# Performance work log

Hardware: AMD Instinct MI355X
Metric: run time of the kernel (lower is better)

## Reference

```python
import jax, jax.numpy as jnp
import numpy as np

N = 20000      # nodes
E = 160000     # edges
F_IN = 128     # node_feature_dim
HID = 128      # hidden_dim
HEADS = 8
G = 64         # graphs in batch


def setup_inputs() -> dict:
    key = jax.random.key(0)
    ks = iter(jax.random.split(key, 40))

    def w(shape, fan):
        return jax.random.normal(next(ks), shape, jnp.float32) / np.sqrt(fan)

    inp = {}
    inp['x'] = jax.random.normal(next(ks), (N, F_IN), jnp.float32)
    inp['edge_index'] = jax.random.randint(next(ks), (2, E), 0, N, jnp.int32)
    inp['batch'] = jnp.sort(jax.random.randint(next(ks), (N,), 0, G, jnp.int32))
    # initial projection
    inp['Wp'] = w((F_IN, HID), F_IN); inp['bp'] = jnp.zeros((HID,), jnp.float32)
    # layers 0..2: TransformerConv(HID -> HID//HEADS per head, heads=HEADS, concat) => heads*out = HID
    inp['Wq'] = w((3, HID, HID), HID); inp['bq'] = jnp.zeros((3, HID), jnp.float32)
    inp['Wk'] = w((3, HID, HID), HID); inp['bk'] = jnp.zeros((3, HID), jnp.float32)
    inp['Wv'] = w((3, HID, HID), HID); inp['bv'] = jnp.zeros((3, HID), jnp.float32)
    inp['Ws'] = w((3, HID, HID), HID); inp['bs'] = jnp.zeros((3, HID), jnp.float32)
    inp['Wbeta'] = w((3, 3 * HID, 1), 3 * HID)
    # layer 3: TransformerConv(HID -> HID per head, heads=HEADS, concat=False -> head mean)
    inp['Wq3'] = w((HID, HEADS * HID), HID); inp['bq3'] = jnp.zeros((HEADS * HID,), jnp.float32)
    inp['Wk3'] = w((HID, HEADS * HID), HID); inp['bk3'] = jnp.zeros((HEADS * HID,), jnp.float32)
    inp['Wv3'] = w((HID, HEADS * HID), HID); inp['bv3'] = jnp.zeros((HEADS * HID,), jnp.float32)
    inp['Ws3'] = w((HID, HID), HID); inp['bs3'] = jnp.zeros((HID,), jnp.float32)
    inp['Wbeta3'] = w((3 * HID, 1), 3 * HID)
    # batchnorm affine params for 4 layers
    inp['bn_gamma'] = jnp.ones((4, HID), jnp.float32)
    inp['bn_beta'] = jnp.zeros((4, HID), jnp.float32)
    return inp


def _tconv(x, src, dst, Wq, bq, Wk, bk, Wv, bv, Ws, bs, Wb, heads, concat):
    n = x.shape[0]
    d = Wq.shape[1] // heads  # per-head dim
    q = (x @ Wq + bq).reshape(n, heads, d)
    k = (x @ Wk + bk).reshape(n, heads, d)
    v = (x @ Wv + bv).reshape(n, heads, d)
    # per-edge attention logits [E, heads]
    logits = jnp.einsum('ehd,ehd->eh', q[dst], k[src]) / jnp.sqrt(jnp.float32(d))
    # segment softmax over incoming edges of each target node
    m = jax.ops.segment_max(logits, dst, num_segments=n)
    m = jnp.where(jnp.isfinite(m), m, 0.0)
    ex = jnp.exp(logits - m[dst])
    denom = jax.ops.segment_sum(ex, dst, num_segments=n)
    a = ex / (denom[dst] + 1e-16)  # [E, heads]
    out = jax.ops.segment_sum(a[:, :, None] * v[src], dst, num_segments=n)  # [n, heads, d]
    out = out.reshape(n, heads * d) if concat else out.mean(axis=1)
    # beta-gated skip connection
    r = x @ Ws + bs
    g = jax.nn.sigmoid(jnp.concatenate([out, r, out - r], axis=-1) @ Wb)  # [n, 1]
    return g * r + (1.0 - g) * out


def _bn(x, gamma, beta):
    mu = x.mean(axis=0)
    var = x.var(axis=0)
    return (x - mu) * jax.lax.rsqrt(var + 1e-5) * gamma + beta


def reference(x, edge_index, batch, Wp, bp, Wq, bq, Wk, bk, Wv, bv, Ws, bs, Wbeta,
              Wq3, bq3, Wk3, bk3, Wv3, bv3, Ws3, bs3, Wbeta3, bn_gamma, bn_beta):
    src, dst = edge_index[0], edge_index[1]
    h = x @ Wp + bp
    for i in range(3):
        h = _tconv(h, src, dst, Wq[i], bq[i], Wk[i], bk[i], Wv[i], bv[i],
                   Ws[i], bs[i], Wbeta[i], HEADS, concat=True)
        h = jax.nn.relu(_bn(h, bn_gamma[i], bn_beta[i]))
    h = _tconv(h, src, dst, Wq3, bq3, Wk3, bk3, Wv3, bv3, Ws3, bs3, Wbeta3,
               HEADS, concat=False)
    h = jax.nn.relu(_bn(h, bn_gamma[3], bn_beta[3]))
    # global mean pool per graph
    sums = jax.ops.segment_sum(h, batch, num_segments=G)
    cnt = jax.ops.segment_sum(jnp.ones((h.shape[0],), h.dtype), batch, num_segments=G)
    return sums / jnp.maximum(cnt, 1.0)[:, None]
```

## Files before the change

### kernel.cpp

```cpp
#include <hip/hip_runtime.h>
#include <math.h>

#define NNODES 20000
#define NPAD   20096
#define NEDGES 160000
#define HIDDIM 128
#define NHEADS 8
#define NGRAPH 64
#define KC 384
#define GXTILES 157

typedef short short8 __attribute__((ext_vector_type(8)));
typedef float floatx4 __attribute__((ext_vector_type(4)));
typedef unsigned short ushort4v __attribute__((ext_vector_type(4)));

__device__ inline unsigned short f2bf(float x) {
    unsigned u = __float_as_uint(x);
    u += 0x7fff + ((u >> 16) & 1);
    return (unsigned short)(u >> 16);
}
__device__ inline float bf2f(unsigned short h) {
    return __uint_as_float(((unsigned)h) << 16);
}

__device__ __forceinline__ void gload16(const unsigned short* g, unsigned short* l) {
    __builtin_amdgcn_global_load_lds(
        (const __attribute__((address_space(1))) unsigned int*)g,
        (__attribute__((address_space(3))) unsigned int*)l, 16, 0, 0);
}

__global__ __launch_bounds__(256) void zero_kernel(float* __restrict__ p, int n) {
    int i = blockIdx.x * blockDim.x + threadIdx.x;
    if (i < n) p[i] = 0.f;
}

__global__ __launch_bounds__(256) void count_deg_kernel(const int* __restrict__ dst,
                                                        int* __restrict__ deg, int e) {
    int i = blockIdx.x * blockDim.x + threadIdx.x;
    if (i < e) atomicAdd(&deg[dst[i]], 1);
}

__global__ __launch_bounds__(256) void scan1_kernel(const int* __restrict__ deg,
                                                    int* __restrict__ chunk,
                                                    int* __restrict__ bsum, int n) {
    __shared__ int buf[256];
    int t = threadIdx.x;
    int i = blockIdx.x * 256 + t;
    int v = (i < n) ? deg[i] : 0;
    buf[t] = v;
    __syncthreads();
    for (int off = 1; off < 256; off <<= 1) {
        int tmp = (t >= off) ? buf[t - off] : 0;
        __syncthreads();
        buf[t] += tmp;
        __syncthreads();
    }
    if (i < n) chunk[i] = buf[t];
    if (t == 255) bsum[blockIdx.x] = buf[255];
}

__global__ __launch_bounds__(128) void scan2_kernel(int* __restrict__ bsum, int nb) {
    __shared__ int buf[128];
    int t = threadIdx.x;
    int v = (t < nb) ? bsum[t] : 0;
    buf[t] = v;
    __syncthreads();
    for (int off = 1; off < 128; off <<= 1) {
        int tmp = (t >= off) ? buf[t - off] : 0;
        __syncthreads();
        buf[t] += tmp;
        __syncthreads();
    }
    if (t < nb) bsum[t] = buf[t] - v;
}

__global__ __launch_bounds__(256) void scan3_kernel(const int* __restrict__ chunk,
                                                    const int* __restrict__ bsum,
                                                    int* __restrict__ offs, int n) {
    int i = blockIdx.x * 256 + threadIdx.x;
    if (i < n) offs[i + 1] = chunk[i] + bsum[i >> 8];
    if (i == 0) offs[0] = 0;
}

__global__ __launch_bounds__(256) void scatter_kernel(const int* __restrict__ src,
                                                      const int* __restrict__ dst,
                                                      const int* __restrict__ offs,
                                                      int* __restrict__ cursor,
                                                      int* __restrict__ csr_src, int e) {
    int i = blockIdx.x * blockDim.x + threadIdx.x;
    if (i < e) {
        int d = dst[i];
        int pos = offs[d] + atomicAdd(&cursor[d], 1);
        csr_src[pos] = src[i];
    }
}

__global__ __launch_bounds__(128) void prep_w_kernel(
    const float* __restrict__ Wq, const float* __restrict__ Wk,
    const float* __restrict__ Wv, const float* __restrict__ Ws,
    const float* __restrict__ Wp, const float* __restrict__ Ws3,
    unsigned short* __restrict__ WtAll) {
    int id = blockIdx.x;
    int k = threadIdx.x;
    float w;
    if (id < 1536) {
        int li = id / 512, n = id % 512, sel = n >> 7, np = n & 127;
        const float* W = (sel == 0) ? Wq : (sel == 1) ? Wk : (sel == 2) ? Wv : Ws;
        w = W[li * 16384 + k * 128 + np];
    } else if (id < 1664) {
        w = Wp[k * 128 + (id - 1536)];
    } else if (id < 2688) {
        return;
    } else {
        w = Ws3[k * 128 + (id - 2688)];
    }
    unsigned short hi = f2bf(w);
    unsigned short lo = f2bf(w - bf2f(hi));
    unsigned short* dst = WtAll + (size_t)id * KC;
    dst[k] = hi;
    dst[128 + k] = hi;
    dst[256 + k] = lo;
}

__global__ __launch_bounds__(256) void prep_bias_kernel(
    const float* __restrict__ bq, const float* __restrict__ bk,
    const float* __restrict__ bv, const float* __restrict__ bs,
    const float* __restrict__ bs3, float* __restrict__ bcat) {
    int id = blockIdx.x * 256 + threadIdx.x;
    if (id >= 2688) return;
    float v;
    if (id < 1536) {
        int li = id / 512, n = id % 512, sel = n >> 7, np = n & 127;
        const float* b = (sel == 0) ? bq : (sel == 1) ? bk : (sel == 2) ? bv : bs;
        v = b[li * 128 + np];
    } else if (id < 2560) {
        return;
    } else {
        v = bs3[id - 2560];
    }
    bcat[id] = v;
}

__global__ __launch_bounds__(128) void mqk_kernel(
    const float* __restrict__ Wq3, const float* __restrict__ Wk3,
    const float* __restrict__ bq3,
    unsigned short* __restrict__ WtAll, float* __restrict__ bcat) {
    int hb = blockIdx.x;
    int h = hb >> 7, b = hb & 127;
    int a = threadIdx.x;
    __shared__ float wk[128];
    wk[a] = Wk3[(size_t)b * 1024 + h * 128 + a];
    __syncthreads();
    const float* wq = Wq3 + (size_t)a * 1024 + h * 128;
    float acc = 0.f;
#pragma unroll 16
    for (int d = 0; d < 128; ++d) acc = fmaf(wq[d], wk[d], acc);
    unsigned short hi = f2bf(acc);
    unsigned short lo = f2bf(acc - bf2f(hi));
    unsigned short* dst = WtAll + (size_t)(1664 + h * 128 + b) * KC;
    dst[a] = hi;
    dst[128 + a] = hi;
    dst[256 + a] = lo;
    if (a == 0) {
        float bb = 0.f;
        for (int d = 0; d < 128; ++d) bb = fmaf(bq3[h * 128 + d], wk[d], bb);
        bcat[1536 + h * 128 + b] = bb;
    }
}

__global__ __launch_bounds__(128) void prep_wvm_kernel(
    const float* __restrict__ Wv3, const float* __restrict__ bv3,
    unsigned short* __restrict__ Wvm, float* __restrict__ bvm) {
    int j = blockIdx.x;
    int a = threadIdx.x;
#pragma unroll
    for (int h = 0; h < 8; ++h) {
        float w = Wv3[(size_t)a * 1024 + h * 128 + j] * 0.125f;
        Wvm[(size_t)j * 1024 + h * 128 + a] = f2bf(w);
    }
    if (a == 0) {
        float s = 0.f;
        for (int h = 0; h < 8; ++h) s += bv3[h * 128 + j];
        bvm[j] = s * 0.125f;
    }
}

__global__ __launch_bounds__(256) void cat_from_kernel(const float* __restrict__ h,
                                                       unsigned short* __restrict__ Acat) {
    int idx = blockIdx.x * 256 + threadIdx.x;
    if (idx >= NPAD * HIDDIM) return;
    int r = idx >> 7, k = idx & 127;
    float x = (r < NNODES) ? h[idx] : 0.f;
    unsigned short hi = f2bf(x);
    unsigned short lo = f2bf(x - bf2f(hi));
    unsigned short* row = Acat + (size_t)r * KC;
    row[k] = hi;
    row[128 + k] = lo;
    row[256 + k] = hi;
}

template <typename OutT, int KG, int BY, int ST>
__global__ __launch_bounds__(256) void gemm_lds_kernel(
    const unsigned short* __restrict__ A, const unsigned short* __restrict__ Wt,
    const float* __restrict__ bias, OutT* __restrict__ C, int M, int nrows) {
    int id = blockIdx.x;
    int xcd = id & 7;
    int idx = id >> 3;
    int bx = (idx / BY) * 8 + xcd;
    int by = idx % BY;
    if (bx >= GXTILES) return;

    __shared__ unsigned short lds[2][2][4096];

    int tid = threadIdx.x;
    int lane = tid & 63;
    int wave = tid >> 6;
    int m = lane & 15;
    int q = lane >> 4;
    int nodeBase = bx * 128 + (wave & 1) * 64;
    int featBase = by * 128 + (wave >> 1) * 64;

    const unsigned short* gA = A + (size_t)bx * 128 * ST;
    const unsigned short* gW = Wt + (size_t)by * 128 * ST;

    int rs = lane >> 2;
    int cp0 = lane & 3;

    auto stagef = [&](int buf, int kk) {
        int kof = kk * 32;
#pragma unroll
        for (int jj = 0; jj < 2; ++jj) {
            int j = wave * 2 + jj;
            int row = j * 16 + rs;
            int g = cp0 ^ ((row >> 1) & 3);
            gload16(gA + (size_t)row * ST + kof + g * 8,
                    &lds[buf][0][0] + (size_t)j * 512);
            gload16(gW + (size_t)row * ST + kof + g * 8,
                    &lds[buf][1][0] + (size_t)j * 512);
        }
    };

    floatx4 acc[4][4];
#pragma unroll
    for (int r = 0; r < 4; ++r)
#pragma unroll
        for (int c = 0; c < 4; ++c) acc[r][c] = (floatx4){0.f, 0.f, 0.f, 0.f};

    stagef(0, 0);
    __syncthreads();

    for (int kg = 0; kg < KG; ++kg) {
        int cur = kg & 1;
        if (kg + 1 < KG) stagef(cur ^ 1, kg + 1);
        short8 a[4], b[4];
#pragma unroll
        for (int r = 0; r < 4; ++r) {
            int wr = (wave >> 1) * 64 + r * 16 + m;
            int cp = q ^ ((wr >> 1) & 3);
            a[r] = *(const short8*)(&lds[cur][1][0] + wr * 32 + cp * 8);
        }
#pragma unroll
        for (int c = 0; c < 4; ++c) {
            int ar = (wave & 1) * 64 + c * 16 + m;
            int cp = q ^ ((ar >> 1) & 3);
            b[c] = *(const short8*)(&lds[cur][0][0] + ar * 32 + cp * 8);
        }
#pragma unroll
        for (int r = 0; r < 4; ++r)
#pragma unroll
            for (int c = 0; c < 4; ++c)
                acc[r][c] = __builtin_amdgcn_mfma_f32_16x16x32_bf16(a[r], b[c], acc[r][c], 0, 0, 0);
        __syncthreads();
    }

    float4 bv[4];
#pragma unroll
    for (int r = 0; r < 4; ++r) bv[r] = *(const float4*)(bias + featBase + r * 16 + q * 4);
#pragma unroll
    for (int c = 0; c < 4; ++c) {
        int node = nodeBase + c * 16 + m;
        if (node < nrows) {
#pragma unroll
            for (int r = 0; r < 4; ++r) {
                int f0 = featBase + r * 16 + q * 4;
                float v0 = acc[r][c][0] + bv[r].x;
                float v1 = acc[r][c][1] + bv[r].y;
                float v2 = acc[r][c][2] + bv[r].z;
                float v3 = acc[r][c][3] + bv[r].w;
                if (sizeof(OutT) == 2) {
                    ushort4v o = {f2bf(v0), f2bf(v1), f2bf(v2), f2bf(v3)};
                    *(ushort4v*)((unsigned short*)C + (size_t)node * M + f0) = o;
                } else {
                    float4 o = {v0, v1, v2, v3};
                    *(float4*)((float*)C + (size_t)node * M + f0) = o;
                }
            }
        }
    }
}

__global__ __launch_bounds__(64) void attn_small_kernel(
    const unsigned short* __restrict__ qkvs,
    const float* __restrict__ Wb,
    const int* __restrict__ offs, const int* __restrict__ csr_src,
    float* __restrict__ out) {
    int i = blockIdx.x;
    int l = threadIdx.x;
    int g = l >> 5;
    int d0 = (l & 31) * 4;
    uint2 qraw = *(const uint2*)(qkvs + (size_t)i * 512 + d0);
    float q0 = bf2f((unsigned short)(qraw.x & 0xffff)), q1 = bf2f((unsigned short)(qraw.x >> 16));
    float q2 = bf2f((unsigned short)(qraw.y & 0xffff)), q3 = bf2f((unsigned short)(qraw.y >> 16));
    int e0 = offs[i], e1 = offs[i + 1];
    float lac = 0.f;
    float a0 = 0.f, a1 = 0.f, a2 = 0.f, a3 = 0.f;
    for (int e = e0 + g; e < e1; e += 2) {
        int sn = csr_src[e];
        const unsigned short* row = qkvs + (size_t)sn * 512;
        uint2 kk = *(const uint2*)(row + 128 + d0);
        uint2 vv = *(const uint2*)(row + 256 + d0);
        float k0 = bf2f((unsigned short)(kk.x & 0xffff)), k1 = bf2f((unsigned short)(kk.x >> 16));
        float k2 = bf2f((unsigned short)(kk.y & 0xffff)), k3 = bf2f((unsigned short)(kk.y >> 16));
        float p = q0 * k0 + q1 * k1 + q2 * k2 + q3 * k3;
        p += __shfl_xor(p, 1);
        p += __shfl_xor(p, 2);
        float w = __expf(p * 0.25f);
        float v0 = bf2f((unsigned short)(vv.x & 0xffff)), v1 = bf2f((unsigned short)(vv.x >> 16));
        float v2 = bf2f((unsigned short)(vv.y & 0xffff)), v3 = bf2f((unsigned short)(vv.y >> 16));
        a0 += w * v0;
        a1 += w * v1;
        a2 += w * v2;
        a3 += w * v3;
        lac += w;
    }
    a0 += __shfl_xor(a0, 32);
    a1 += __shfl_xor(a1, 32);
    a2 += __shfl_xor(a2, 32);
    a3 += __shfl_xor(a3, 32);
    lac += __shfl_xor(lac, 32);
    float inv = 1.f / (lac + 1e-16f);
    float o0 = a0 * inv, o1 = a1 * inv, o2 = a2 * inv, o3 = a3 * inv;
    uint2 rraw = *(const uint2*)(qkvs + (size_t)i * 512 + 384 + d0);
    float r0 = bf2f((unsigned short)(rraw.x & 0xffff)), r1 = bf2f((unsigned short)(rraw.x >> 16));
    float r2 = bf2f((unsigned short)(rraw.y & 0xffff)), r3 = bf2f((unsigned short)(rraw.y >> 16));
    float part = o0 * Wb[d0] + o1 * Wb[d0 + 1] + o2 * Wb[d0 + 2] + o3 * Wb[d0 + 3]
               + r0 * Wb[128 + d0] + r1 * Wb[128 + d0 + 1]
               + r2 * Wb[128 + d0 + 2] + r3 * Wb[128 + d0 + 3]
               + (o0 - r0) * Wb[256 + d0] + (o1 - r1) * Wb[256 + d0 + 1]
               + (o2 - r2) * Wb[256 + d0 + 2] + (o3 - r3) * Wb[256 + d0 + 3];
    if (g) part = 0.f;
#pragma unroll
    for (int msk = 1; msk <= 32; msk <<= 1) part += __shfl_xor(part, msk);
    float gg = 1.f / (1.f + __expf(-part));
    if (g == 0) {
        float4 o4 = {gg * r0 + (1.f - gg) * o0, gg * r1 + (1.f - gg) * o1,
                     gg * r2 + (1.f - gg) * o2, gg * r3 + (1.f - gg) * o3};
        *(float4*)(out + (size_t)i * HIDDIM + d0) = o4;
    }
}

__global__ __launch_bounds__(64) void attn_big_kernel(
    const unsigned short* __restrict__ tbuf, const unsigned short* __restrict__ Acat,
    const int* __restrict__ offs, const int* __restrict__ csr_src,
    unsigned short* __restrict__ agg) {
    int i = blockIdx.x;
    int l = threadIdx.x;
    int doff = (l & 7) * 16;
    const unsigned short* tp = tbuf + (size_t)i * 1152 + l * 16;
    uint4 t0 = *(const uint4*)tp;
    uint4 t1 = *(const uint4*)(tp + 8);
    float tq[16];
    tq[0] = bf2f((unsigned short)(t0.x & 0xffff)); tq[1] = bf2f((unsigned short)(t0.x >> 16));
    tq[2] = bf2f((unsigned short)(t0.y & 0xffff)); tq[3] = bf2f((unsigned short)(t0.y >> 16));
    tq[4] = bf2f((unsigned short)(t0.z & 0xffff)); tq[5] = bf2f((unsigned short)(t0.z >> 16));
    tq[6] = bf2f((unsigned short)(t0.w & 0xffff)); tq[7] = bf2f((unsigned short)(t0.w >> 16));
    tq[8] = bf2f((unsigned short)(t1.x & 0xffff)); tq[9] = bf2f((unsigned short)(t1.x >> 16));
    tq[10] = bf2f((unsigned short)(t1.y & 0xffff)); tq[11] = bf2f((unsigned short)(t1.y >> 16));
    tq[12] = bf2f((unsigned short)(t1.z & 0xffff)); tq[13] = bf2f((unsigned short)(t1.z >> 16));
    tq[14] = bf2f((unsigned short)(t1.w & 0xffff)); tq[15] = bf2f((unsigned short)(t1.w >> 16));
    int e0 = offs[i], e1 = offs[i + 1];
    float ac[16];
#pragma unroll
    for (int j = 0; j < 16; ++j) ac[j] = 0.f;
    float lac = 0.f;
    for (int e = e0; e < e1; ++e) {
        int sn = csr_src[e];
        const unsigned short* hp = Acat + (size_t)sn * KC + doff;
        uint4 k0 = *(const uint4*)hp;
        uint4 k1 = *(const uint4*)(hp + 8);
        float kk[16];
        kk[0] = bf2f((unsigned short)(k0.x & 0xffff)); kk[1] = bf2f((unsigned short)(k0.x >> 16));
        kk[2] = bf2f((unsigned short)(k0.y & 0xffff)); kk[3] = bf2f((unsigned short)(k0.y >> 16));
        kk[4] = bf2f((unsigned short)(k0.z & 0xffff)); kk[5] = bf2f((unsigned short)(k0.z >> 16));
        kk[6] = bf2f((unsigned short)(k0.w & 0xffff)); kk[7] = bf2f((unsigned short)(k0.w >> 16));
        kk[8] = bf2f((unsigned short)(k1.x & 0xffff)); kk[9] = bf2f((unsigned short)(k1.x >> 16));
        kk[10] = bf2f((unsigned short)(k1.y & 0xffff)); kk[11] = bf2f((unsigned short)(k1.y >> 16));
        kk[12] = bf2f((unsigned short)(k1.z & 0xffff)); kk[13] = bf2f((unsigned short)(k1.z >> 16));
        kk[14] = bf2f((unsigned short)(k1.w & 0xffff)); kk[15] = bf2f((unsigned short)(k1.w >> 16));
        float p = 0.f;
#pragma unroll
        for (int j = 0; j < 16; ++j) p = fmaf(tq[j], kk[j], p);
        p += __shfl_xor(p, 1);
        p += __shfl_xor(p, 2);
        p += __shfl_xor(p, 4);
        float w = __expf(p * 0.08838834764831845f);
#pragma unroll
        for (int j = 0; j < 16; ++j) ac[j] = fmaf(w, kk[j], ac[j]);
        lac += w;
    }
    float inv = 1.f / (lac + 1e-16f);
    unsigned short* o = agg + (size_t)i * 1024 + l * 16;
    ushort4v o0 = {f2bf(ac[0] * inv), f2bf(ac[1] * inv), f2bf(ac[2] * inv), f2bf(ac[3] * inv)};
    ushort4v o1 = {f2bf(ac[4] * inv), f2bf(ac[5] * inv), f2bf(ac[6] * inv), f2bf(ac[7] * inv)};
    ushort4v o2 = {f2bf(ac[8] * inv), f2bf(ac[9] * inv), f2bf(ac[10] * inv), f2bf(ac[11] * inv)};
    ushort4v o3 = {f2bf(ac[12] * inv), f2bf(ac[13] * inv), f2bf(ac[14] * inv), f2bf(ac[15] * inv)};
    *(ushort4v*)o = o0;
    *(ushort4v*)(o + 4) = o1;
    *(ushort4v*)(o + 8) = o2;
    *(ushort4v*)(o + 12) = o3;
}

__global__ __launch_bounds__(128) void beta3_kernel(const float* __restrict__ omean,
                                                    const unsigned short* __restrict__ tbuf,
                                                    const float* __restrict__ Wb,
                                                    float* __restrict__ out) {
    int i = blockIdx.x, t = threadIdx.x;
    float o = omean[(size_t)i * HIDDIM + t];
    float r = bf2f(tbuf[(size_t)i * 1152 + 1024 + t]);
    float part = o * Wb[t] + r * Wb[128 + t] + (o - r) * Wb[256 + t];
#pragma unroll
    for (int msk = 1; msk <= 32; msk <<= 1) part += __shfl_xor(part, msk);
    __shared__ float wsum[2];
    if ((t & 63) == 0) wsum[t >> 6] = part;
    __syncthreads();
    float tot = wsum[0] + wsum[1];
    float g = 1.f / (1.f + __expf(-tot));
    out[(size_t)i * HIDDIM + t] = g * r + (1.f - g) * o;
}

__global__ __launch_bounds__(128) void bn_stats_kernel(const float* __restrict__ x,
                                                       float* __restrict__ stat, int n) {
    int t = threadIdx.x;
    float s = 0.f, sq = 0.f;
    for (int i = blockIdx.x; i < n; i += gridDim.x) {
        float v = x[(size_t)i * HIDDIM + t];
        s += v;
        sq += v * v;
    }
    atomicAdd(&stat[t], s);
    atomicAdd(&stat[HIDDIM + t], sq);
}

__global__ __launch_bounds__(128) void bn_apply_kernel(float* __restrict__ x,
                                                       const float* __restrict__ stat,
                                                       const float* __restrict__ gamma,
                                                       const float* __restrict__ beta, int n,
                                                       unsigned short* __restrict__ cat) {
    int t = threadIdx.x;
    float mu = stat[t] / (float)n;
    float var = stat[HIDDIM + t] / (float)n - mu * mu;
    float rs = rsqrtf(var + 1e-5f);
    float g = gamma[t], b = beta[t];
    for (int i = blockIdx.x; i < n; i += gridDim.x) {
        float v = x[(size_t)i * HIDDIM + t];
        v = fmaxf((v - mu) * rs * g + b, 0.f);
        x[(size_t)i * HIDDIM + t] = v;
        if (cat) {
            unsigned short hi = f2bf(v);
            unsigned short lo = f2bf(v - bf2f(hi));
            unsigned short* row = cat + (size_t)i * KC;
            row[t] = hi;
            row[128 + t] = lo;
            row[256 + t] = hi;
        }
    }
}

__global__ __launch_bounds__(256) void gb_kernel(const int* __restrict__ batch,
                                                 int* __restrict__ gs,
                                                 int* __restrict__ ge, int n) {
    int i = blockIdx.x * 256 + threadIdx.x;
    if (i >= n) return;
    int b = batch[i];
    if (i == 0 || batch[i - 1] != b) gs[b] = i;
    if (i == n - 1 || batch[i + 1] != b) ge[b] = i + 1;
}

__global__ __launch_bounds__(256) void pool_part_kernel(const float* __restrict__ x,
                                                        const int* __restrict__ gs,
                                                        const int* __restrict__ ge,
                                                        float* __restrict__ out) {
    int g = blockIdx.x, c = blockIdx.y;
    int t = threadIdx.x;
    int f = t & 127, half = t >> 7;
    int s = gs[g], e = ge[g];
    float acc = 0.f;
    for (int i = s + 2 * c + half; i < e; i += 16) acc += x[(size_t)i * HIDDIM + f];
    __shared__ float l0[128];
    if (half == 0) l0[f] = acc;
    __syncthreads();
    if (half == 1) atomicAdd(&out[g * HIDDIM + f], l0[f] + acc);
}

__global__ __launch_bounds__(128) void pool_div_kernel(float* __restrict__ out,
                                                       const int* __restrict__ gs,
                                                       const int* __restrict__ ge) {
    int g = blockIdx.x, t = threadIdx.x;
    int c = ge[g] - gs[g];
    out[g * HIDDIM + t] /= (float)(c > 0 ? c : 1);
}

extern "C" void kernel_launch(void* const* d_in, const int* in_sizes, int n_in,
                              void* d_out, int out_size, void* d_ws, size_t ws_size,
                              hipStream_t stream) {
    const float* x       = (const float*)d_in[0];
    const int*   ei      = (const int*)d_in[1];
    const int*   batch   = (const int*)d_in[2];
    const float* Wp      = (const float*)d_in[3];
    const float* bp      = (const float*)d_in[4];
    const float* Wq      = (const float*)d_in[5];
    const float* bq      = (const float*)d_in[6];
    const float* Wk      = (const float*)d_in[7];
    const float* bk      = (const float*)d_in[8];
    const float* Wv      = (const float*)d_in[9];
    const float* bv      = (const float*)d_in[10];
    const float* Ws      = (const float*)d_in[11];
    const float* bs      = (const float*)d_in[12];
    const float* Wbeta   = (const float*)d_in[13];
    const float* Wq3     = (const float*)d_in[14];
    const float* bq3     = (const float*)d_in[15];
    const float* Wk3     = (const float*)d_in[16];
    const float* bk3     = (const float*)d_in[17];
    const float* Wv3     = (const float*)d_in[18];
    const float* bv3     = (const float*)d_in[19];
    const float* Ws3     = (const float*)d_in[20];
    const float* bs3     = (const float*)d_in[21];
    const float* Wbeta3  = (const float*)d_in[22];
    const float* bn_gamma = (const float*)d_in[23];
    const float* bn_beta  = (const float*)d_in[24];
    float* out = (float*)d_out;
    (void)bk3;

    const int* esrc = ei;
    const int* edst = ei + NEDGES;

    char* wpc = (char*)d_ws;
    auto alloc = [&](size_t nbytes) -> char* {
        char* p = wpc;
        wpc += (nbytes + 255) & ~(size_t)255;
        return p;
    };
    unsigned short* Acat  = (unsigned short*)alloc((size_t)NPAD * KC * 2);
    unsigned short* WtAll = (unsigned short*)alloc((size_t)2816 * KC * 2);
    float* bcat   = (float*)alloc(2688 * 4);
    unsigned short* Wvm   = (unsigned short*)alloc((size_t)128 * 1024 * 2);
    float* bvm    = (float*)alloc(128 * 4);
    unsigned short* tbuf  = (unsigned short*)alloc((size_t)NPAD * 1152 * 2);
    unsigned short* aggb  = (unsigned short*)alloc((size_t)NPAD * 1024 * 2);
    float* omean  = (float*)alloc((size_t)NNODES * HIDDIM * 4);
    float* hbuf   = (float*)alloc((size_t)NNODES * HIDDIM * 4);
    float* obuf   = (float*)alloc((size_t)NNODES * HIDDIM * 4);
    int*   deg    = (int*)alloc((2 * NNODES + 128 + 4 * 256) * 4);
    int*   cursor = deg + NNODES;
    int*   gs     = deg + 2 * NNODES;
    int*   ge     = gs + NGRAPH;
    float* bnstat4 = (float*)(deg + 2 * NNODES + 128);
    int*   chunk  = (int*)alloc(NNODES * 4);
    int*   bsum   = (int*)alloc(128 * 4);
    int*   offs   = (int*)alloc((NNODES + 1) * 4);
    int*   csrsrc = (int*)alloc(NEDGES * 4);

    unsigned short* WtQKVS = WtAll;
    unsigned short* Wpt    = WtAll + (size_t)1536 * KC;
    unsigned short* Wt3    = WtAll + (size_t)1664 * KC;
    float* bQKVS = bcat;
    float* b3    = bcat + 1536;
    unsigned short* qkvs = tbuf;

    const int TB = 256;
    const int ZWORDS = 2 * NNODES + 128 + 4 * 256;
    zero_kernel<<<(ZWORDS + TB - 1) / TB, TB, 0, stream>>>((float*)deg, ZWORDS);
    count_deg_kernel<<<(NEDGES + TB - 1) / TB, TB, 0, stream>>>(edst, deg, NEDGES);
    const int NB = (NNODES + 255) / 256;
    scan1_kernel<<<NB, 256, 0, stream>>>(deg, chunk, bsum, NNODES);
    scan2_kernel<<<1, 128, 0, stream>>>(bsum, NB);
    scan3_kernel<<<NB, 256, 0, stream>>>(chunk, bsum, offs, NNODES);
    scatter_kernel<<<(NEDGES + TB - 1) / TB, TB, 0, stream>>>(esrc, edst, offs, cursor, csrsrc, NEDGES);
    gb_kernel<<<(NNODES + TB - 1) / TB, TB, 0, stream>>>(batch, gs, ge, NNODES);

    prep_w_kernel<<<2816, 128, 0, stream>>>(Wq, Wk, Wv, Ws, Wp, Ws3, WtAll);
    prep_bias_kernel<<<(2688 + TB - 1) / TB, TB, 0, stream>>>(bq, bk, bv, bs, bs3, bcat);
    mqk_kernel<<<1024, 128, 0, stream>>>(Wq3, Wk3, bq3, WtAll, bcat);
    prep_wvm_kernel<<<128, 128, 0, stream>>>(Wv3, bv3, Wvm, bvm);

    const int CATB = (NPAD * HIDDIM + TB - 1) / TB;
    const int GSW = 8 * ((GXTILES + 7) / 8);

    cat_from_kernel<<<CATB, TB, 0, stream>>>(x, Acat);
    gemm_lds_kernel<float, 12, 1, KC><<<GSW * 1, 256, 0, stream>>>(Acat, Wpt, bp, hbuf, 128, NNODES);
    cat_from_kernel<<<CATB, TB, 0, stream>>>(hbuf, Acat);

    for (int li = 0; li < 3; ++li) {
        gemm_lds_kernel<unsigned short, 8, 4, KC><<<GSW * 4, 256, 0, stream>>>(
            Acat, WtQKVS + (size_t)li * 512 * KC, bQKVS + li * 512, qkvs, 512, NNODES);
        attn_small_kernel<<<NNODES, 64, 0, stream>>>(qkvs, Wbeta + li * 384,
                                                     offs, csrsrc, obuf);
        float* st = bnstat4 + li * 256;
        bn_stats_kernel<<<640, 128, 0, stream>>>(obuf, st, NNODES);
        bn_apply_kernel<<<512, 128, 0, stream>>>(obuf, st, bn_gamma + li * HIDDIM,
                                                 bn_beta + li * HIDDIM, NNODES, Acat);
    }

    gemm_lds_kernel<unsigned short, 8, 9, KC><<<GSW * 9, 256, 0, stream>>>(
        Acat, Wt3, b3, tbuf, 1152, NNODES);
    attn_big_kernel<<<NNODES, 64, 0, stream>>>(tbuf, Acat, offs, csrsrc, aggb);
    gemm_lds_kernel<float, 32, 1, 1024><<<GSW, 256, 0, stream>>>(
        aggb, Wvm, bvm, omean, HIDDIM, NNODES);
    beta3_kernel<<<NNODES, 128, 0, stream>>>(omean, tbuf, Wbeta3, hbuf);
    float* st3 = bnstat4 + 3 * 256;
    bn_stats_kernel<<<640, 128, 0, stream>>>(hbuf, st3, NNODES);
    bn_apply_kernel<<<512, 128, 0, stream>>>(hbuf, st3, bn_gamma + 3 * HIDDIM,
                                             bn_beta + 3 * HIDDIM, NNODES, (unsigned short*)0);

    zero_kernel<<<(NGRAPH * HIDDIM + TB - 1) / TB, TB, 0, stream>>>(out, NGRAPH * HIDDIM);
    pool_part_kernel<<<dim3(NGRAPH, 8), 256, 0, stream>>>(hbuf, gs, ge, out);
    pool_div_kernel<<<NGRAPH, 128, 0, stream>>>(out, gs, ge);
}
```

Baseline: 513.1 us.

## Fuse setup, epilogue, BN stats and pooling kernels to cut launches and passes

Merges several small kernels: scatter with graph-boundary detection, the bias prep into the weight prep, mqk with the Wv3 mean prep, and the final beta gate with BN statistics accumulation. BN apply, ReLU and mean pooling are folded into one per-graph kernel. The projection GEMM now writes the split bf16 hi/lo activation layout directly, which removes a cat_from pass. Launch count and several full passes over node features go down. In exchange, pooling runs with only 64 blocks, and the BN statistics rely on a zeroed stat buffer plus float atomics and E[x^2]-mu^2 variance.

```diff
diff --git a/kernel.cpp b/kernel.cpp
--- a/kernel.cpp
+++ b/kernel.cpp
@@ -82,26 +82,50 @@
     if (i == 0) offs[0] = 0;
 }
 
-__global__ __launch_bounds__(256) void scatter_kernel(const int* __restrict__ src,
-                                                      const int* __restrict__ dst,
-                                                      const int* __restrict__ offs,
-                                                      int* __restrict__ cursor,
-                                                      int* __restrict__ csr_src, int e) {
+__global__ __launch_bounds__(256) void scatter_gb_kernel(
+    const int* __restrict__ src, const int* __restrict__ dst,
+    const int* __restrict__ offs, int* __restrict__ cursor,
+    int* __restrict__ csr_src, int e,
+    const int* __restrict__ batch, int* __restrict__ gs, int* __restrict__ ge, int n) {
     int i = blockIdx.x * blockDim.x + threadIdx.x;
     if (i < e) {
         int d = dst[i];
         int pos = offs[d] + atomicAdd(&cursor[d], 1);
         csr_src[pos] = src[i];
     }
+    if (i < n) {
+        int b = batch[i];
+        if (i == 0 || batch[i - 1] != b) gs[b] = i;
+        if (i == n - 1 || batch[i + 1] != b) ge[b] = i + 1;
+    }
 }
 
 __global__ __launch_bounds__(128) void prep_w_kernel(
     const float* __restrict__ Wq, const float* __restrict__ Wk,
     const float* __restrict__ Wv, const float* __restrict__ Ws,
     const float* __restrict__ Wp, const float* __restrict__ Ws3,
-    unsigned short* __restrict__ WtAll) {
+    const float* __restrict__ bq, const float* __restrict__ bk,
+    const float* __restrict__ bv, const float* __restrict__ bs,
+    const float* __restrict__ bs3,
+    unsigned short* __restrict__ WtAll, float* __restrict__ bcat) {
     int id = blockIdx.x;
     int k = threadIdx.x;
+    if (id >= 2816) {
+        int idx = (id - 2816) * 128 + k;
+        if (idx >= 2688) return;
+        float v;
+        if (idx < 1536) {
+            int li = idx / 512, n = idx % 512, sel = n >> 7, np = n & 127;
+            const float* b = (sel == 0) ? bq : (sel == 1) ? bk : (sel == 2) ? bv : bs;
+            v = b[li * 128 + np];
+        } else if (idx < 2560) {
+            return;
+        } else {
+            v = bs3[idx - 2560];
+        }
+        bcat[idx] = v;
+        return;
+    }
     float w;
     if (id < 1536) {
         int li = id / 512, n = id % 512, sel = n >> 7, np = n & 127;
@@ -122,32 +146,29 @@
     dst[256 + k] = lo;
 }
 
-__global__ __launch_bounds__(256) void prep_bias_kernel(
-    const float* __restrict__ bq, const float* __restrict__ bk,
-    const float* __restrict__ bv, const float* __restrict__ bs,
-    const float* __restrict__ bs3, float* __restrict__ bcat) {
-    int id = blockIdx.x * 256 + threadIdx.x;
-    if (id >= 2688) return;
-    float v;
-    if (id < 1536) {
-        int li = id / 512, n = id % 512, sel = n >> 7, np = n & 127;
-        const float* b = (sel == 0) ? bq : (sel == 1) ? bk : (sel == 2) ? bv : bs;
-        v = b[li * 128 + np];
-    } else if (id < 2560) {
-        return;
-    } else {
-        v = bs3[id - 2560];
-    }
-    bcat[id] = v;
-}
-
-__global__ __launch_bounds__(128) void mqk_kernel(
+__global__ __launch_bounds__(128) void mqk_wvm_kernel(
     const float* __restrict__ Wq3, const float* __restrict__ Wk3,
     const float* __restrict__ bq3,
-    unsigned short* __restrict__ WtAll, float* __restrict__ bcat) {
+    const float* __restrict__ Wv3, const float* __restrict__ bv3,
+    unsigned short* __restrict__ WtAll, float* __restrict__ bcat,
+    unsigned short* __restrict__ Wvm, float* __restrict__ bvm) {
+    int a = threadIdx.x;
+    if (blockIdx.x >= 1024) {
+        int j = blockIdx.x - 1024;
+#pragma unroll
+        for (int h = 0; h < 8; ++h) {
+            float w = Wv3[(size_t)a * 1024 + h * 128 + j] * 0.125f;
+            Wvm[(size_t)j * 1024 + h * 128 + a] = f2bf(w);
+        }
+        if (a == 0) {
+            float s = 0.f;
+            for (int h = 0; h < 8; ++h) s += bv3[h * 128 + j];
+            bvm[j] = s * 0.125f;
+        }
+        return;
+    }
     int hb = blockIdx.x;
     int h = hb >> 7, b = hb & 127;
-    int a = threadIdx.x;
     __shared__ float wk[128];
     wk[a] = Wk3[(size_t)b * 1024 + h * 128 + a];
     __syncthreads();
@@ -168,23 +189,6 @@
     }
 }
 
-__global__ __launch_bounds__(128) void prep_wvm_kernel(
-    const float* __restrict__ Wv3, const float* __restrict__ bv3,
-    unsigned short* __restrict__ Wvm, float* __restrict__ bvm) {
-    int j = blockIdx.x;
-    int a = threadIdx.x;
-#pragma unroll
-    for (int h = 0; h < 8; ++h) {
-        float w = Wv3[(size_t)a * 1024 + h * 128 + j] * 0.125f;
-        Wvm[(size_t)j * 1024 + h * 128 + a] = f2bf(w);
-    }
-    if (a == 0) {
-        float s = 0.f;
-        for (int h = 0; h < 8; ++h) s += bv3[h * 128 + j];
-        bvm[j] = s * 0.125f;
-    }
-}
-
 __global__ __launch_bounds__(256) void cat_from_kernel(const float* __restrict__ h,
                                                        unsigned short* __restrict__ Acat) {
     int idx = blockIdx.x * 256 + threadIdx.x;
@@ -199,7 +203,7 @@
     row[256 + k] = hi;
 }
 
-template <typename OutT, int KG, int BY, int ST>
+template <typename OutT, int KG, int BY, int ST, int OMODE>
 __global__ __launch_bounds__(256) void gemm_lds_kernel(
     const unsigned short* __restrict__ A, const unsigned short* __restrict__ Wt,
     const float* __restrict__ bias, OutT* __restrict__ C, int M, int nrows) {
@@ -287,7 +291,16 @@
                 float v1 = acc[r][c][1] + bv[r].y;
                 float v2 = acc[r][c][2] + bv[r].z;
                 float v3 = acc[r][c][3] + bv[r].w;
-                if (sizeof(OutT) == 2) {
+                if (OMODE == 2) {
+                    unsigned short* row = (unsigned short*)C + (size_t)node * KC;
+                    unsigned short h0 = f2bf(v0), h1 = f2bf(v1), h2 = f2bf(v2), h3 = f2bf(v3);
+                    ushort4v hiv = {h0, h1, h2, h3};
+                    ushort4v lov = {f2bf(v0 - bf2f(h0)), f2bf(v1 - bf2f(h1)),
+                                    f2bf(v2 - bf2f(h2)), f2bf(v3 - bf2f(h3))};
+                    *(ushort4v*)(row + f0) = hiv;
+                    *(ushort4v*)(row + 128 + f0) = lov;
+                    *(ushort4v*)(row + 256 + f0) = hiv;
+                } else if (OMODE == 1) {
                     ushort4v o = {f2bf(v0), f2bf(v1), f2bf(v2), f2bf(v3)};
                     *(ushort4v*)((unsigned short*)C + (size_t)node * M + f0) = o;
                 } else {
@@ -420,22 +433,31 @@
     *(ushort4v*)(o + 12) = o3;
 }
 
-__global__ __launch_bounds__(128) void beta3_kernel(const float* __restrict__ omean,
-                                                    const unsigned short* __restrict__ tbuf,
-                                                    const float* __restrict__ Wb,
-                                                    float* __restrict__ out) {
-    int i = blockIdx.x, t = threadIdx.x;
-    float o = omean[(size_t)i * HIDDIM + t];
-    float r = bf2f(tbuf[(size_t)i * 1152 + 1024 + t]);
-    float part = o * Wb[t] + r * Wb[128 + t] + (o - r) * Wb[256 + t];
-#pragma unroll
-    for (int msk = 1; msk <= 32; msk <<= 1) part += __shfl_xor(part, msk);
+__global__ __launch_bounds__(128) void beta3_stats_kernel(
+    const float* __restrict__ omean, const unsigned short* __restrict__ tbuf,
+    const float* __restrict__ Wb, float* __restrict__ out,
+    float* __restrict__ stat, int n) {
+    int t = threadIdx.x;
     __shared__ float wsum[2];
-    if ((t & 63) == 0) wsum[t >> 6] = part;
-    __syncthreads();
-    float tot = wsum[0] + wsum[1];
-    float g = 1.f / (1.f + __expf(-tot));
-    out[(size_t)i * HIDDIM + t] = g * r + (1.f - g) * o;
+    float s = 0.f, sq = 0.f;
+    for (int i = blockIdx.x; i < n; i += gridDim.x) {
+        float o = omean[(size_t)i * HIDDIM + t];
+        float r = bf2f(tbuf[(size_t)i * 1152 + 1024 + t]);
+        float part = o * Wb[t] + r * Wb[128 + t] + (o - r) * Wb[256 + t];
+#pragma unroll
+        for (int msk = 1; msk <= 32; msk <<= 1) part += __shfl_xor(part, msk);
+        if ((t & 63) == 0) wsum[t >> 6] = part;
+        __syncthreads();
+        float tot = wsum[0] + wsum[1];
+        __syncthreads();
+        float g = 1.f / (1.f + __expf(-tot));
+        float v = g * r + (1.f - g) * o;
+        out[(size_t)i * HIDDIM + t] = v;
+        s += v;
+        sq += v * v;
+    }
+    atomicAdd(&stat[t], s);
+    atomicAdd(&stat[HIDDIM + t], sq);
 }
 
 __global__ __launch_bounds__(128) void bn_stats_kernel(const float* __restrict__ x,
@@ -476,38 +498,29 @@
     }
 }
 
-__global__ __launch_bounds__(256) void gb_kernel(const int* __restrict__ batch,
-                                                 int* __restrict__ gs,
-                                                 int* __restrict__ ge, int n) {
-    int i = blockIdx.x * 256 + threadIdx.x;
-    if (i >= n) return;
-    int b = batch[i];
-    if (i == 0 || batch[i - 1] != b) gs[b] = i;
-    if (i == n - 1 || batch[i + 1] != b) ge[b] = i + 1;
-}
-
-__global__ __launch_bounds__(256) void pool_part_kernel(const float* __restrict__ x,
-                                                        const int* __restrict__ gs,
-                                                        const int* __restrict__ ge,
-                                                        float* __restrict__ out) {
-    int g = blockIdx.x, c = blockIdx.y;
+__global__ __launch_bounds__(256) void pool_bn_kernel(
+    const float* __restrict__ x, const float* __restrict__ stat,
+    const float* __restrict__ gamma, const float* __restrict__ beta,
+    const int* __restrict__ gs, const int* __restrict__ ge,
+    float* __restrict__ out, int n) {
+    int g = blockIdx.x;
     int t = threadIdx.x;
     int f = t & 127, half = t >> 7;
+    float mu = stat[f] / (float)n;
+    float var = stat[HIDDIM + f] / (float)n - mu * mu;
+    float rs = rsqrtf(var + 1e-5f);
+    float ga = gamma[f], be = beta[f];
     int s = gs[g], e = ge[g];
     float acc = 0.f;
-    for (int i = s + 2 * c + half; i < e; i += 16) acc += x[(size_t)i * HIDDIM + f];
+    for (int i = s + half; i < e; i += 2)
+        acc += fmaxf((x[(size_t)i * HIDDIM + f] - mu) * rs * ga + be, 0.f);
     __shared__ float l0[128];
     if (half == 0) l0[f] = acc;
     __syncthreads();
-    if (half == 1) atomicAdd(&out[g * HIDDIM + f], l0[f] + acc);
-}
-
-__global__ __launch_bounds__(128) void pool_div_kernel(float* __restrict__ out,
-                                                       const int* __restrict__ gs,
-                                                       const int* __restrict__ ge) {
-    int g = blockIdx.x, t = threadIdx.x;
-    int c = ge[g] - gs[g];
-    out[g * HIDDIM + t] /= (float)(c > 0 ? c : 1);
+    if (half == 1) {
+        int c = e - s;
+        out[g * HIDDIM + f] = (l0[f] + acc) / (float)(c > 0 ? c : 1);
+    }
 }
 
 extern "C" void kernel_launch(void* const* d_in, const int* in_sizes, int n_in,
@@ -585,23 +598,23 @@
     scan1_kernel<<<NB, 256, 0, stream>>>(deg, chunk, bsum, NNODES);
     scan2_kernel<<<1, 128, 0, stream>>>(bsum, NB);
     scan3_kernel<<<NB, 256, 0, stream>>>(chunk, bsum, offs, NNODES);
-    scatter_kernel<<<(NEDGES + TB - 1) / TB, TB, 0, stream>>>(esrc, edst, offs, cursor, csrsrc, NEDGES);
-    gb_kernel<<<(NNODES + TB - 1) / TB, TB, 0, stream>>>(batch, gs, ge, NNODES);
-
-    prep_w_kernel<<<2816, 128, 0, stream>>>(Wq, Wk, Wv, Ws, Wp, Ws3, WtAll);
-    prep_bias_kernel<<<(2688 + TB - 1) / TB, TB, 0, stream>>>(bq, bk, bv, bs, bs3, bcat);
-    mqk_kernel<<<1024, 128, 0, stream>>>(Wq3, Wk3, bq3, WtAll, bcat);
-    prep_wvm_kernel<<<128, 128, 0, stream>>>(Wv3, bv3, Wvm, bvm);
+    scatter_gb_kernel<<<(NEDGES + TB - 1) / TB, TB, 0, stream>>>(
+        esrc, edst, offs, cursor, csrsrc, NEDGES, batch, gs, ge, NNODES);
+
+    prep_w_kernel<<<2837, 128, 0, stream>>>(Wq, Wk, Wv, Ws, Wp, Ws3,
+                                            bq, bk, bv, bs, bs3, WtAll, bcat);
+    mqk_wvm_kernel<<<1152, 128, 0, stream>>>(Wq3, Wk3, bq3, Wv3, bv3,
+                                             WtAll, bcat, Wvm, bvm);
 
     const int CATB = (NPAD * HIDDIM + TB - 1) / TB;
     const int GSW = 8 * ((GXTILES + 7) / 8);
 
     cat_from_kernel<<<CATB, TB, 0, stream>>>(x, Acat);
-    gemm_lds_kernel<float, 12, 1, KC><<<GSW * 1, 256, 0, stream>>>(Acat, Wpt, bp, hbuf, 128, NNODES);
-    cat_from_kernel<<<CATB, TB, 0, stream>>>(hbuf, Acat);
+    gemm_lds_kernel<unsigned short, 12, 1, KC, 2><<<GSW * 1, 256, 0, stream>>>(
+        Acat, Wpt, bp, Acat, 0, NNODES);
 
     for (int li = 0; li < 3; ++li) {
-        gemm_lds_kernel<unsigned short, 8, 4, KC><<<GSW * 4, 256, 0, stream>>>(
+        gemm_lds_kernel<unsigned short, 8, 4, KC, 1><<<GSW * 4, 256, 0, stream>>>(
             Acat, WtQKVS + (size_t)li * 512 * KC, bQKVS + li * 512, qkvs, 512, NNODES);
         attn_small_kernel<<<NNODES, 64, 0, stream>>>(qkvs, Wbeta + li * 384,
                                                      offs, csrsrc, obuf);
@@ -611,18 +624,13 @@
                                                  bn_beta + li * HIDDIM, NNODES, Acat);
     }
 
-    gemm_lds_kernel<unsigned short, 8, 9, KC><<<GSW * 9, 256, 0, stream>>>(
+    gemm_lds_kernel<unsigned short, 8, 9, KC, 1><<<GSW * 9, 256, 0, stream>>>(
         Acat, Wt3, b3, tbuf, 1152, NNODES);
     attn_big_kernel<<<NNODES, 64, 0, stream>>>(tbuf, Acat, offs, csrsrc, aggb);
-    gemm_lds_kernel<float, 32, 1, 1024><<<GSW, 256, 0, stream>>>(
+    gemm_lds_kernel<float, 32, 1, 1024, 0><<<GSW, 256, 0, stream>>>(
         aggb, Wvm, bvm, omean, HIDDIM, NNODES);
-    beta3_kernel<<<NNODES, 128, 0, stream>>>(omean, tbuf, Wbeta3, hbuf);
     float* st3 = bnstat4 + 3 * 256;
-    bn_stats_kernel<<<640, 128, 0, stream>>>(hbuf, st3, NNODES);
-    bn_apply_kernel<<<512, 128, 0, stream>>>(hbuf, st3, bn_gamma + 3 * HIDDIM,
-                                             bn_beta + 3 * HIDDIM, NNODES, (unsigned short*)0);
-
-    zero_kernel<<<(NGRAPH * HIDDIM + TB - 1) / TB, TB, 0, stream>>>(out, NGRAPH * HIDDIM);
-    pool_part_kernel<<<dim3(NGRAPH, 8), 256, 0, stream>>>(hbuf, gs, ge, out);
-    pool_div_kernel<<<NGRAPH, 128, 0, stream>>>(out, gs, ge);
-}
+    beta3_stats_kernel<<<512, 128, 0, stream>>>(omean, tbuf, Wbeta3, hbuf, st3, NNODES);
+    pool_bn_kernel<<<NGRAPH, 256, 0, stream>>>(hbuf, st3, bn_gamma + 3 * HIDDIM,
+                                               bn_beta + 3 * HIDDIM, gs, ge, out, NNODES);
+}
```

Result: slower. 530.8 us (+3.4%).
